# Performance work log

Measured on AMD Instinct MI355X. Metric: run time of the kernel, lower is better.

Reference implementation:

```python
import jax, jax.numpy as jnp
import numpy as np

B, S, DIM, NH = 2, 2048, 1536, 12
HD = DIM // NH            # 128
C = HD // 2               # 64 rotary pairs
CF = C - 2 * (C // 3)     # 22 (frame axis)
CH = C // 3               # 21 (height axis)
CW = C // 3               # 21 (width axis)
GF, GH, GW = 8, 16, 16    # grid sizes, GF*GH*GW == S
EPS = 1e-6


def _freq_table(n_pos, dim):
    inv = 1.0 / (10000.0 ** (np.arange(dim, dtype=np.float64) / dim))
    ang = np.outer(np.arange(n_pos, dtype=np.float64), inv)
    return (np.cos(ang).astype(np.float32), np.sin(ang).astype(np.float32))


def setup_inputs() -> dict:
    key = jax.random.key(0)
    ks = jax.random.split(key, 8)
    scale = 0.02
    cos_f, sin_f = _freq_table(GF, CF)
    cos_h, sin_h = _freq_table(GH, CH)
    cos_w, sin_w = _freq_table(GW, CW)
    return {
        'x': jax.random.normal(ks[0], (B, S, DIM), dtype=jnp.float32),
        'seq_lens': jnp.array([2048, 1600], dtype=jnp.int32),
        'f': GF, 'h': GH, 'w': GW,
        'wq': scale * jax.random.normal(ks[1], (DIM, DIM), dtype=jnp.float32),
        'bq': jnp.zeros((DIM,), jnp.float32),
        'wk': scale * jax.random.normal(ks[2], (DIM, DIM), dtype=jnp.float32),
        'bk': jnp.zeros((DIM,), jnp.float32),
        'wv': scale * jax.random.normal(ks[3], (DIM, DIM), dtype=jnp.float32),
        'bv': jnp.zeros((DIM,), jnp.float32),
        'wo': scale * jax.random.normal(ks[4], (DIM, DIM), dtype=jnp.float32),
        'bo': jnp.zeros((DIM,), jnp.float32),
        'nq_w': jnp.ones((DIM,), jnp.float32),
        'nk_w': jnp.ones((DIM,), jnp.float32),
        'cos_f': jnp.asarray(cos_f), 'sin_f': jnp.asarray(sin_f),
        'cos_h': jnp.asarray(cos_h), 'sin_h': jnp.asarray(sin_h),
        'cos_w': jnp.asarray(cos_w), 'sin_w': jnp.asarray(sin_w),
    }


def _rmsnorm(t, wt):
    return t * jax.lax.rsqrt(jnp.mean(t * t, axis=-1, keepdims=True) + EPS) * wt


def _grid_rope(t, cos, sin, b, s):
    # t: [b, s, NH, HD] ; cos/sin: [s, 1, C] (per-position assembled freqs)
    tp = t.reshape(b, s, NH, C, 2)
    xr, xi = tp[..., 0], tp[..., 1]
    rr = xr * cos - xi * sin          # complex multiply by e^{i*theta}
    ri = xr * sin + xi * cos
    return jnp.stack([rr, ri], axis=-1).reshape(b, s, NH, HD)


def reference(x, seq_lens, f, h, w, wq, bq, wk, bk, wv, bv, wo, bo,
              nq_w, nk_w, cos_f, sin_f, cos_h, sin_h, cos_w, sin_w):
    b, s, _ = x.shape
    # QKV projections with RMSNorm on q/k over full dim (as in the module)
    q = _rmsnorm(x @ wq.T + bq, nq_w).reshape(b, s, NH, HD)
    k = _rmsnorm(x @ wk.T + bk, nk_w).reshape(b, s, NH, HD)
    v = (x @ wv.T + bv).reshape(b, s, NH, HD)
    # grid-indexed RoPE: zero offsets / target==grid => arange sampling per axis
    idx = jnp.arange(s)
    fi = idx // (h * w)
    hi = (idx // w) % h
    wi = idx % w
    cos = jnp.concatenate([cos_f[fi], cos_h[hi], cos_w[wi]], axis=-1)[:, None, :]
    sin = jnp.concatenate([sin_f[fi], sin_h[hi], sin_w[wi]], axis=-1)[:, None, :]
    qr = _grid_rope(q, cos, sin, b, s)
    kr = _grid_rope(k, cos, sin, b, s)
    # attention with ragged key-length masking (flash_attention k_lens)
    scale = 1.0 / jnp.sqrt(jnp.float32(HD))
    scores = jnp.einsum('bqnd,bknd->bnqk', qr, kr) * scale
    kmask = idx[None, :] < seq_lens[:, None]            # [b, s]
    scores = jnp.where(kmask[:, None, None, :], scores, jnp.float32(-1e30))
    attn = jax.nn.softmax(scores, axis=-1)
    out = jnp.einsum('bnqk,bknd->bqnd', attn, v).reshape(b, s, DIM)
    return out @ wo.T + bo
```

## Files before the change

### kernel.cpp

```cpp
#include <hip/hip_runtime.h>
#include <hip/hip_bf16.h>
#include <math.h>

#define DIM_  1536
#define NH_   12
#define HD_   128
#define S_    2048
#define B_    2
#define M_    (B_*S_)
#define WEL_  (DIM_*DIM_)

typedef __attribute__((ext_vector_type(8))) _Float16 f16x8;
typedef __attribute__((ext_vector_type(4))) short short4v;
typedef __attribute__((ext_vector_type(8))) short short8v;
typedef __attribute__((ext_vector_type(4))) float f32x4;

#define SSCALE_LOG2E (0.08838834764831845f * 1.4426950408889634f)

static __device__ __forceinline__ short f2h(float f) {
  union { _Float16 h; short s; } u;
  u.h = (_Float16)f;
  return u.s;
}

static __device__ __forceinline__ unsigned pk2h(float a, float b) {
  typedef __attribute__((ext_vector_type(2))) __fp16 fp16x2;
  union { fp16x2 v; unsigned u; } u2;
  u2.v = __builtin_amdgcn_cvt_pkrtz(a, b);
  return u2.u;
}

__global__ __launch_bounds__(256) void f2h_k(
    const float* __restrict__ in, short* __restrict__ out, int n8)
{
  int i = blockIdx.x * 256 + threadIdx.x;
  if (i >= n8) return;
  const float4* p = (const float4*)in + (size_t)i * 2;
  float4 a = p[0], b = p[1];
  short8v o;
  o[0] = f2h(a.x); o[1] = f2h(a.y); o[2] = f2h(a.z); o[3] = f2h(a.w);
  o[4] = f2h(b.x); o[5] = f2h(b.y); o[6] = f2h(b.z); o[7] = f2h(b.w);
  *((short8v*)out + i) = o;
}

__global__ __launch_bounds__(256) void f2h4_k(
    const float* __restrict__ x, const float* __restrict__ wq,
    const float* __restrict__ wk, const float* __restrict__ wv,
    short* __restrict__ x16, short* __restrict__ w16)
{
  int i = blockIdx.x * 256 + threadIdx.x;
  const float* src; short* dst; int j;
  if (i < 786432)       { src = x;  dst = x16;            j = i; }
  else if (i < 1081344) { src = wq; dst = w16;            j = i - 786432; }
  else if (i < 1376256) { src = wk; dst = w16 + WEL_;     j = i - 1081344; }
  else                  { src = wv; dst = w16 + 2 * WEL_; j = i - 1376256; }
  const float4* p = (const float4*)src + (size_t)j * 2;
  float4 a = p[0], b = p[1];
  short8v o;
  o[0] = f2h(a.x); o[1] = f2h(a.y); o[2] = f2h(a.z); o[3] = f2h(a.w);
  o[4] = f2h(b.x); o[5] = f2h(b.y); o[6] = f2h(b.z); o[7] = f2h(b.w);
  *((short8v*)dst + j) = o;
}

template<int MODE>
static __device__ __forceinline__ void gemm16_core(
    const short* __restrict__ A16, const short* __restrict__ W16,
    const float* __restrict__ bias, short* __restrict__ Outp,
    int m0, int n0)
{
  __shared__ __align__(16) char Atile[8192];
  __shared__ __align__(16) char Btile[8192];
  const int tid = threadIdx.x;
  const int l  = tid & 63, w = tid >> 6;
  const int wr = w >> 1, wc = w & 1;
  const int lc = l & 15, lg = l >> 4;

  f32x4 acc[4][4] = {};

  const int rs  = w * 16 + (l >> 2);
  const int gsl = ((l & 3) ^ ((rs >> 1) & 3)) * 8;
  const short* gA0 = A16 + (size_t)(m0 + rs) * DIM_ + gsl;
  const short* gA1 = A16 + (size_t)(m0 + 64 + rs) * DIM_ + gsl;
  const short* gB0 = W16 + (size_t)(n0 + rs) * DIM_ + gsl;
  const short* gB1 = W16 + (size_t)(n0 + 64 + rs) * DIM_ + gsl;

  for (int k0 = 0; k0 < DIM_; k0 += 32) {
    __builtin_amdgcn_global_load_lds(
        (const __attribute__((address_space(1))) unsigned*)(gA0 + k0),
        (__attribute__((address_space(3))) unsigned*)(Atile + w * 1024), 16, 0, 0);
    __builtin_amdgcn_global_load_lds(
        (const __attribute__((address_space(1))) unsigned*)(gA1 + k0),
        (__attribute__((address_space(3))) unsigned*)(Atile + 4096 + w * 1024), 16, 0, 0);
    __builtin_amdgcn_global_load_lds(
        (const __attribute__((address_space(1))) unsigned*)(gB0 + k0),
        (__attribute__((address_space(3))) unsigned*)(Btile + w * 1024), 16, 0, 0);
    __builtin_amdgcn_global_load_lds(
        (const __attribute__((address_space(1))) unsigned*)(gB1 + k0),
        (__attribute__((address_space(3))) unsigned*)(Btile + 4096 + w * 1024), 16, 0, 0);
    __syncthreads();

    f16x8 af[4], bf[4];
#pragma unroll
    for (int mt = 0; mt < 4; ++mt) {
      int ar = wr * 64 + mt * 16 + lc;
      af[mt] = *(const f16x8*)(Atile + ar * 64 + ((lg ^ ((ar >> 1) & 3)) << 4));
    }
#pragma unroll
    for (int nt = 0; nt < 4; ++nt) {
      int br = wc * 64 + nt * 16 + lc;
      bf[nt] = *(const f16x8*)(Btile + br * 64 + ((lg ^ ((br >> 1) & 3)) << 4));
    }
#pragma unroll
    for (int mt = 0; mt < 4; ++mt)
#pragma unroll
      for (int nt = 0; nt < 4; ++nt)
        acc[mt][nt] = __builtin_amdgcn_mfma_f32_16x16x32_f16(af[mt], bf[nt], acc[mt][nt], 0, 0, 0);
    __syncthreads();
  }

  if (MODE == 0) {
#pragma unroll
    for (int nt = 0; nt < 4; ++nt) {
      int col = n0 + wc * 64 + nt * 16 + lc;
      float bb = bias[col];
#pragma unroll
      for (int mt = 0; mt < 4; ++mt) {
#pragma unroll
        for (int r = 0; r < 4; ++r) {
          int rowm = m0 + wr * 64 + mt * 16 + lg * 4 + r;
          Outp[(size_t)rowm * DIM_ + col] = f2h(acc[mt][nt][r] + bb);
        }
      }
    }
  } else {
#pragma unroll
    for (int nt = 0; nt < 4; ++nt) {
      int colg = n0 + wc * 64 + nt * 16 + lc;
      int h = colg >> 7, d = colg & 127;
      float bb = bias[colg];
#pragma unroll
      for (int mt = 0; mt < 4; ++mt) {
        int rowg = m0 + wr * 64 + mt * 16 + lg * 4;
        int b = rowg >> 11, s = rowg & (S_ - 1);
        short4v o4;
#pragma unroll
        for (int r = 0; r < 4; ++r) o4[r] = f2h(acc[mt][nt][r] + bb);
        *(short4v*)(Outp + ((size_t)((b * NH_ + h) * HD_ + d)) * S_ + s) = o4;
      }
    }
  }
}

__global__ __launch_bounds__(256) void gemm_qkv16_k(
    const short* __restrict__ x16, const short* __restrict__ w16,
    const float* __restrict__ bq, const float* __restrict__ bk,
    const float* __restrict__ bv,
    short* __restrict__ q16, short* __restrict__ k16, short* __restrict__ vt)
{
  const int z = blockIdx.z;
  if (z == 2)
    gemm16_core<2>(x16, w16 + 2 * (size_t)WEL_, bv, vt,
                   blockIdx.y * 128, blockIdx.x * 128);
  else
    gemm16_core<0>(x16, w16 + (size_t)z * WEL_, z ? bk : bq, z ? k16 : q16,
                   blockIdx.y * 128, blockIdx.x * 128);
}

__global__ __launch_bounds__(256) void gemm_out64_k(
    const short* __restrict__ att16, const short* __restrict__ wo16,
    const float* __restrict__ bo, float* __restrict__ out)
{
  __shared__ __align__(16) char Atile[8192];
  __shared__ __align__(16) char Btile[4096];
  const int m0 = blockIdx.y * 128, n0 = blockIdx.x * 64;
  const int tid = threadIdx.x;
  const int l  = tid & 63, w = tid >> 6;
  const int lc = l & 15, lg = l >> 4;

  f32x4 acc[2][4] = {};

  const int rsA = w * 32 + (l >> 2);
  const int rsB = w * 16 + (l >> 2);
  const int gslA = ((l & 3) ^ ((rsA >> 1) & 3)) * 8;
  const int gslB = ((l & 3) ^ ((rsB >> 1) & 3)) * 8;
  const short* gA0 = att16 + (size_t)(m0 + rsA) * DIM_ + gslA;
  const short* gA1 = att16 + (size_t)(m0 + 16 + rsA) * DIM_ + gslA;
  const short* gB0 = wo16 + (size_t)(n0 + rsB) * DIM_ + gslB;

  for (int k0 = 0; k0 < DIM_; k0 += 32) {
    __builtin_amdgcn_global_load_lds(
        (const __attribute__((address_space(1))) unsigned*)(gA0 + k0),
        (__attribute__((address_space(3))) unsigned*)(Atile + w * 2048), 16, 0, 0);
    __builtin_amdgcn_global_load_lds(
        (const __attribute__((address_space(1))) unsigned*)(gA1 + k0),
        (__attribute__((address_space(3))) unsigned*)(Atile + w * 2048 + 1024), 16, 0, 0);
    __builtin_amdgcn_global_load_lds(
        (const __attribute__((address_space(1))) unsigned*)(gB0 + k0),
        (__attribute__((address_space(3))) unsigned*)(Btile + w * 1024), 16, 0, 0);
    __syncthreads();

    f16x8 af[2], bf[4];
#pragma unroll
    for (int mt = 0; mt < 2; ++mt) {
      int ar = w * 32 + mt * 16 + lc;
      af[mt] = *(const f16x8*)(Atile + ar * 64 + ((lg ^ ((ar >> 1) & 3)) << 4));
    }
#pragma unroll
    for (int nt = 0; nt < 4; ++nt) {
      int br = nt * 16 + lc;
      bf[nt] = *(const f16x8*)(Btile + br * 64 + ((lg ^ ((br >> 1) & 3)) << 4));
    }
#pragma unroll
    for (int mt = 0; mt < 2; ++mt)
#pragma unroll
      for (int nt = 0; nt < 4; ++nt)
        acc[mt][nt] = __builtin_amdgcn_mfma_f32_16x16x32_f16(af[mt], bf[nt], acc[mt][nt], 0, 0, 0);
    __syncthreads();
  }

#pragma unroll
  for (int nt = 0; nt < 4; ++nt) {
    int col = n0 + nt * 16 + lc;
    float bb = bo[col];
#pragma unroll
    for (int mt = 0; mt < 2; ++mt) {
#pragma unroll
      for (int r = 0; r < 4; ++r) {
        int rowm = m0 + w * 32 + mt * 16 + lg * 4 + r;
        out[(size_t)rowm * DIM_ + col] = acc[mt][nt][r] + bb;
      }
    }
  }
}

__global__ __launch_bounds__(256) void rms_rope_pack16_k(
    const short* __restrict__ t, const float* __restrict__ w,
    const float* __restrict__ cf, const float* __restrict__ sf,
    const float* __restrict__ ch, const float* __restrict__ sh,
    const float* __restrict__ cw, const float* __restrict__ sw,
    short* __restrict__ outb, float qsc)
{
  const int row = blockIdx.x;
  const int b   = row >> 11;
  const int s   = row & (S_ - 1);
  const _Float16* rp = (const _Float16*)(t + (size_t)row * DIM_);

  float ss = 0.f;
  for (int i = threadIdx.x; i < DIM_; i += 256) {
    float v2 = (float)rp[i]; ss += v2 * v2;
  }
#pragma unroll
  for (int off = 32; off > 0; off >>= 1) ss += __shfl_down(ss, off);
  __shared__ float red[4];
  if ((threadIdx.x & 63) == 0) red[threadIdx.x >> 6] = ss;
  __syncthreads();
  float scale = rsqrtf((red[0] + red[1] + red[2] + red[3]) * (1.f / DIM_) + 1e-6f) * qsc;

  const int fi = s >> 8;
  const int hi = (s >> 4) & 15;
  const int wi = s & 15;

  for (int p = threadIdx.x; p < NH_ * 64; p += 256) {
    int n = p >> 6, c = p & 63;
    float co, si;
    if (c < 22)      { co = cf[fi * 22 + c];        si = sf[fi * 22 + c]; }
    else if (c < 43) { co = ch[hi * 21 + (c - 22)]; si = sh[hi * 21 + (c - 22)]; }
    else             { co = cw[wi * 21 + (c - 43)]; si = sw[wi * 21 + (c - 43)]; }
    int d0 = n * HD_ + 2 * c;
    float xr = (float)rp[d0]     * scale * w[d0];
    float xi = (float)rp[d0 + 1] * scale * w[d0 + 1];
    float rr = xr * co - xi * si;
    float ri = xr * si + xi * co;
    *(unsigned int*)(outb + (((size_t)(b * NH_ + n) * S_ + s) * HD_ + 2 * c)) = pk2h(rr, ri);
  }
}

__global__ __launch_bounds__(256) void attn_mfma5_k(
    const short* __restrict__ qb, const short* __restrict__ kb,
    const short* __restrict__ vtb, const int* __restrict__ seq_lens,
    short* __restrict__ o16)
{
  const int bh = blockIdx.y;
  const int b  = bh / NH_;
  const int h  = bh - b * NH_;
  const int q0 = blockIdx.x << 6;
  const int kvlen = seq_lens[b];
  const int tid  = threadIdx.x;
  const int wid  = tid >> 6;
  const int lane = tid & 63;
  const int lg   = lane >> 4;
  const int lc   = lane & 15;
  const int xo   = (lc & 7) << 4;

  __shared__ __align__(16) char Kt[16384];
  __shared__ __align__(16) char Vt[16384];
  __shared__ __align__(16) char Pt[4][2048];

  f16x8 bq[4];
  {
    const size_t base = ((size_t)bh * S_ + q0 + wid * 16 + lc) * HD_;
#pragma unroll
    for (int dc = 0; dc < 4; ++dc)
      bq[dc] = *(const f16x8*)(qb + base + dc * 32 + lg * 8);
  }

  const short* kgA = kb + ((size_t)bh * S_ + wid * 16 + lg) * HD_
                        + ((lc * 8) ^ (lg << 3));
  const short* kgB = kb + ((size_t)bh * S_ + wid * 16 + 4 + lg) * HD_
                        + ((lc * 8) ^ ((lg ^ 4) << 3));
  const short* vg  = vtb + ((size_t)bh * HD_ + wid * 32 + (lane >> 3)) * S_
                         + (((lane & 7) * 8) ^ ((lane >> 3) << 3));

#define STAGE_K()                                                              \
  {                                                                            \
    _Pragma("unroll")                                                          \
    for (int j = 0; j < 4; ++j) {                                              \
      const short* g = (j & 1) ? (kgB + ((j - 1) >> 1) * (8 * HD_))            \
                               : (kgA + (j >> 1) * (8 * HD_));                 \
      __builtin_amdgcn_global_load_lds(                                        \
          (const __attribute__((address_space(1))) unsigned*)g,                \
          (__attribute__((address_space(3))) unsigned*)(Kt + (wid * 16 + j * 4) * 256), \
          16, 0, 0);                                                           \
    }                                                                          \
  }
#define STAGE_V()                                                              \
  {                                                                            \
    _Pragma("unroll")                                                          \
    for (int j = 0; j < 4; ++j) {                                              \
      __builtin_amdgcn_global_load_lds(                                        \
          (const __attribute__((address_space(1))) unsigned*)(vg + j * 8 * S_),\
          (__attribute__((address_space(3))) unsigned*)(Vt + (wid * 32 + j * 8) * 128), \
          16, 0, 0);                                                           \
    }                                                                          \
  }

  f32x4 oacc[8] = {};
  float m = -3.0e38f, l = 0.f;

  const int nt = kvlen >> 6;

  STAGE_K();
  kgA += 64 * HD_; kgB += 64 * HD_;
  __syncthreads();

  for (int ti = 0; ti < nt; ++ti) {
    STAGE_V();
    vg += 64;

    f32x4 s[4];
    __builtin_amdgcn_s_setprio(1);
#pragma unroll
    for (int kt = 0; kt < 4; ++kt) {
      f32x4 a = {0.f, 0.f, 0.f, 0.f};
      const char* kr = Kt + (kt * 16 + lc) * 256;
#pragma unroll
      for (int dc = 0; dc < 4; ++dc) {
        f16x8 kf = *(const f16x8*)(kr + ((dc * 64 + lg * 16) ^ xo));
        a = __builtin_amdgcn_mfma_f32_16x16x32_f16(kf, bq[dc], a, 0, 0, 0);
      }
      s[kt] = a;
    }
    __builtin_amdgcn_s_setprio(0);

    float t0 = -3.0e38f;
#pragma unroll
    for (int kt = 0; kt < 4; ++kt)
#pragma unroll
      for (int r = 0; r < 4; ++r) t0 = fmaxf(t0, s[kt][r]);
    t0 = fmaxf(t0, __shfl_xor(t0, 16));
    t0 = fmaxf(t0, __shfl_xor(t0, 32));

    if (__any(t0 > m + 8.f)) {
      float mn = fmaxf(m, t0);
      float a  = exp2f(m - mn);
      m = mn; l *= a;
#pragma unroll
      for (int r = 0; r < 4; ++r) {
        float ar = __shfl(a, 4 * lg + r);
#pragma unroll
        for (int n = 0; n < 8; ++n) oacc[n][r] *= ar;
      }
    }
    float ls = 0.f;
#pragma unroll
    for (int kt = 0; kt < 4; ++kt)
#pragma unroll
      for (int r = 0; r < 4; ++r) {
        float p = exp2f(s[kt][r] - m); s[kt][r] = p; ls += p;
      }
    ls += __shfl_xor(ls, 16);
    ls += __shfl_xor(ls, 32);
    l += ls;

    {
      char* pr = Pt[wid] + lc * 128;
#pragma unroll
      for (int kt = 0; kt < 4; ++kt) {
#pragma unroll
        for (int rr = 0; rr < 2; ++rr) {
          unsigned u = pk2h(s[kt][2 * rr], s[kt][2 * rr + 1]);
          int off = (kt * 32 + lg * 8 + rr * 4) ^ xo;
          *(unsigned*)(pr + off) = u;
        }
      }
    }

    __syncthreads();

    if (ti + 1 < nt) {
      STAGE_K();
      kgA += 64 * HD_; kgB += 64 * HD_;
    }

    __builtin_amdgcn_s_setprio(1);
#pragma unroll
    for (int kc = 0; kc < 2; ++kc) {
      f16x8 pa = *(const f16x8*)(Pt[wid] + lc * 128 + ((kc * 64 + lg * 16) ^ xo));
#pragma unroll
      for (int n = 0; n < 8; ++n) {
        f16x8 vf = *(const f16x8*)(Vt + (n * 16 + lc) * 128 + ((kc * 64 + lg * 16) ^ xo));
        oacc[n] = __builtin_amdgcn_mfma_f32_16x16x32_f16(pa, vf, oacc[n], 0, 0, 0);
      }
    }
    __builtin_amdgcn_s_setprio(0);

    __syncthreads();
  }

#pragma unroll
  for (int r = 0; r < 4; ++r) {
    float li = 1.f / __shfl(l, 4 * lg + r);
    int qrow = q0 + wid * 16 + 4 * lg + r;
#pragma unroll
    for (int n = 0; n < 8; ++n)
      o16[((size_t)(b * S_ + qrow) * NH_ + h) * HD_ + n * 16 + lc] = f2h(oacc[n][r] * li);
  }
#undef STAGE_K
#undef STAGE_V
}

extern "C" void kernel_launch(void* const* d_in, const int* in_sizes, int n_in,
                              void* d_out, int out_size, void* d_ws, size_t ws_size,
                              hipStream_t stream) {
  const float* x        = (const float*)d_in[0];
  const int*   seq_lens = (const int*)d_in[1];
  const float* wq = (const float*)d_in[5];
  const float* bq = (const float*)d_in[6];
  const float* wk = (const float*)d_in[7];
  const float* bk = (const float*)d_in[8];
  const float* wv = (const float*)d_in[9];
  const float* bv = (const float*)d_in[10];
  const float* wo = (const float*)d_in[11];
  const float* bo = (const float*)d_in[12];
  const float* nq = (const float*)d_in[13];
  const float* nk = (const float*)d_in[14];
  const float* cf = (const float*)d_in[15];
  const float* sf = (const float*)d_in[16];
  const float* ch = (const float*)d_in[17];
  const float* sh = (const float*)d_in[18];
  const float* cw = (const float*)d_in[19];
  const float* sw = (const float*)d_in[20];

  const size_t rowelems = (size_t)M_ * DIM_;
  short* x16 = (short*)d_ws;
  short* w16 = x16 + rowelems;
  short* q16 = w16 + 3 * (size_t)WEL_;
  short* k16 = q16 + rowelems;
  short* vt  = k16 + rowelems;
  short* qh  = vt + rowelems;
  short* kh  = qh + rowelems;
  short* att16 = q16;
  short* wo16  = k16;
  float* out = (float*)d_out;

  f2h4_k<<<6528, 256, 0, stream>>>(x, wq, wk, wv, x16, w16);

  gemm_qkv16_k<<<dim3(DIM_ / 128, M_ / 128, 3), 256, 0, stream>>>(
      x16, w16, bq, bk, bv, q16, k16, vt);

  rms_rope_pack16_k<<<M_, 256, 0, stream>>>(q16, nq, cf, sf, ch, sh, cw, sw, qh,
                                            SSCALE_LOG2E);
  rms_rope_pack16_k<<<M_, 256, 0, stream>>>(k16, nk, cf, sf, ch, sh, cw, sw, kh, 1.0f);

  f2h_k<<<1152, 256, 0, stream>>>(wo, wo16, WEL_ / 8);

  attn_mfma5_k<<<dim3(S_ / 64, B_ * NH_), 256, 0, stream>>>(qh, kh, vt, seq_lens, att16);

  gemm_out64_k<<<dim3(DIM_ / 64, M_ / 128), 256, 0, stream>>>(att16, wo16, bo, out);
}
```

Baseline: 257.0 us.

## Double-buffer LDS tiles in GEMM kernels and fold wo conversion into one launch

Both the QKV and output-projection GEMMs now keep two LDS buffers and prefetch the next K-slice while MFMAs run on the current one. The MFMA block is wrapped in s_setprio to favour math issue. The separate wo fp16 conversion kernel is merged into the combined conversion launch, and wo16 gets its own workspace slot instead of reusing k16. This hides global-load latency and removes one launch, at the cost of doubled LDS per block, which may lower occupancy, and a larger workspace.

```diff
diff --git a/kernel.cpp b/kernel.cpp
--- a/kernel.cpp
+++ b/kernel.cpp
@@ -30,30 +30,19 @@
   return u2.u;
 }
 
-__global__ __launch_bounds__(256) void f2h_k(
-    const float* __restrict__ in, short* __restrict__ out, int n8)
-{
-  int i = blockIdx.x * 256 + threadIdx.x;
-  if (i >= n8) return;
-  const float4* p = (const float4*)in + (size_t)i * 2;
-  float4 a = p[0], b = p[1];
-  short8v o;
-  o[0] = f2h(a.x); o[1] = f2h(a.y); o[2] = f2h(a.z); o[3] = f2h(a.w);
-  o[4] = f2h(b.x); o[5] = f2h(b.y); o[6] = f2h(b.z); o[7] = f2h(b.w);
-  *((short8v*)out + i) = o;
-}
-
-__global__ __launch_bounds__(256) void f2h4_k(
+__global__ __launch_bounds__(256) void f2h5_k(
     const float* __restrict__ x, const float* __restrict__ wq,
     const float* __restrict__ wk, const float* __restrict__ wv,
-    short* __restrict__ x16, short* __restrict__ w16)
+    const float* __restrict__ wo,
+    short* __restrict__ x16, short* __restrict__ w16, short* __restrict__ wo16)
 {
   int i = blockIdx.x * 256 + threadIdx.x;
   const float* src; short* dst; int j;
   if (i < 786432)       { src = x;  dst = x16;            j = i; }
   else if (i < 1081344) { src = wq; dst = w16;            j = i - 786432; }
   else if (i < 1376256) { src = wk; dst = w16 + WEL_;     j = i - 1081344; }
-  else                  { src = wv; dst = w16 + 2 * WEL_; j = i - 1376256; }
+  else if (i < 1671168) { src = wv; dst = w16 + 2 * WEL_; j = i - 1376256; }
+  else                  { src = wo; dst = wo16;           j = i - 1671168; }
   const float4* p = (const float4*)src + (size_t)j * 2;
   float4 a = p[0], b = p[1];
   short8v o;
@@ -66,10 +55,8 @@
 static __device__ __forceinline__ void gemm16_core(
     const short* __restrict__ A16, const short* __restrict__ W16,
     const float* __restrict__ bias, short* __restrict__ Outp,
-    int m0, int n0)
+    int m0, int n0, char* __restrict__ Ab, char* __restrict__ Bb)
 {
-  __shared__ __align__(16) char Atile[8192];
-  __shared__ __align__(16) char Btile[8192];
   const int tid = threadIdx.x;
   const int l  = tid & 63, w = tid >> 6;
   const int wr = w >> 1, wc = w & 1;
@@ -84,39 +71,51 @@
   const short* gB0 = W16 + (size_t)(n0 + rs) * DIM_ + gsl;
   const short* gB1 = W16 + (size_t)(n0 + 64 + rs) * DIM_ + gsl;
 
+#define GSTAGE(buf, k0)                                                        \
+  {                                                                            \
+    __builtin_amdgcn_global_load_lds(                                          \
+        (const __attribute__((address_space(1))) unsigned*)(gA0 + (k0)),       \
+        (__attribute__((address_space(3))) unsigned*)(Ab + (buf) * 8192 + w * 1024), 16, 0, 0); \
+    __builtin_amdgcn_global_load_lds(                                          \
+        (const __attribute__((address_space(1))) unsigned*)(gA1 + (k0)),       \
+        (__attribute__((address_space(3))) unsigned*)(Ab + (buf) * 8192 + 4096 + w * 1024), 16, 0, 0); \
+    __builtin_amdgcn_global_load_lds(                                          \
+        (const __attribute__((address_space(1))) unsigned*)(gB0 + (k0)),       \
+        (__attribute__((address_space(3))) unsigned*)(Bb + (buf) * 8192 + w * 1024), 16, 0, 0); \
+    __builtin_amdgcn_global_load_lds(                                          \
+        (const __attribute__((address_space(1))) unsigned*)(gB1 + (k0)),       \
+        (__attribute__((address_space(3))) unsigned*)(Bb + (buf) * 8192 + 4096 + w * 1024), 16, 0, 0); \
+  }
+
+  GSTAGE(0, 0);
+  __syncthreads();
+  int cur = 0;
   for (int k0 = 0; k0 < DIM_; k0 += 32) {
-    __builtin_amdgcn_global_load_lds(
-        (const __attribute__((address_space(1))) unsigned*)(gA0 + k0),
-        (__attribute__((address_space(3))) unsigned*)(Atile + w * 1024), 16, 0, 0);
-    __builtin_amdgcn_global_load_lds(
-        (const __attribute__((address_space(1))) unsigned*)(gA1 + k0),
-        (__attribute__((address_space(3))) unsigned*)(Atile + 4096 + w * 1024), 16, 0, 0);
-    __builtin_amdgcn_global_load_lds(
-        (const __attribute__((address_space(1))) unsigned*)(gB0 + k0),
-        (__attribute__((address_space(3))) unsigned*)(Btile + w * 1024), 16, 0, 0);
-    __builtin_amdgcn_global_load_lds(
-        (const __attribute__((address_space(1))) unsigned*)(gB1 + k0),
-        (__attribute__((address_space(3))) unsigned*)(Btile + 4096 + w * 1024), 16, 0, 0);
-    __syncthreads();
-
+    const char* Ac = Ab + cur * 8192;
+    const char* Bc = Bb + cur * 8192;
     f16x8 af[4], bf[4];
 #pragma unroll
     for (int mt = 0; mt < 4; ++mt) {
       int ar = wr * 64 + mt * 16 + lc;
-      af[mt] = *(const f16x8*)(Atile + ar * 64 + ((lg ^ ((ar >> 1) & 3)) << 4));
+      af[mt] = *(const f16x8*)(Ac + ar * 64 + ((lg ^ ((ar >> 1) & 3)) << 4));
     }
 #pragma unroll
     for (int nt = 0; nt < 4; ++nt) {
       int br = wc * 64 + nt * 16 + lc;
-      bf[nt] = *(const f16x8*)(Btile + br * 64 + ((lg ^ ((br >> 1) & 3)) << 4));
-    }
+      bf[nt] = *(const f16x8*)(Bc + br * 64 + ((lg ^ ((br >> 1) & 3)) << 4));
+    }
+    if (k0 + 32 < DIM_) GSTAGE(cur ^ 1, k0 + 32);
+    __builtin_amdgcn_s_setprio(1);
 #pragma unroll
     for (int mt = 0; mt < 4; ++mt)
 #pragma unroll
       for (int nt = 0; nt < 4; ++nt)
         acc[mt][nt] = __builtin_amdgcn_mfma_f32_16x16x32_f16(af[mt], bf[nt], acc[mt][nt], 0, 0, 0);
+    __builtin_amdgcn_s_setprio(0);
     __syncthreads();
-  }
+    cur ^= 1;
+  }
+#undef GSTAGE
 
   if (MODE == 0) {
 #pragma unroll
@@ -157,21 +156,23 @@
     const float* __restrict__ bv,
     short* __restrict__ q16, short* __restrict__ k16, short* __restrict__ vt)
 {
+  __shared__ __align__(16) char Ab[2][8192];
+  __shared__ __align__(16) char Bb[2][8192];
   const int z = blockIdx.z;
   if (z == 2)
     gemm16_core<2>(x16, w16 + 2 * (size_t)WEL_, bv, vt,
-                   blockIdx.y * 128, blockIdx.x * 128);
+                   blockIdx.y * 128, blockIdx.x * 128, &Ab[0][0], &Bb[0][0]);
   else
     gemm16_core<0>(x16, w16 + (size_t)z * WEL_, z ? bk : bq, z ? k16 : q16,
-                   blockIdx.y * 128, blockIdx.x * 128);
+                   blockIdx.y * 128, blockIdx.x * 128, &Ab[0][0], &Bb[0][0]);
 }
 
 __global__ __launch_bounds__(256) void gemm_out64_k(
     const short* __restrict__ att16, const short* __restrict__ wo16,
     const float* __restrict__ bo, float* __restrict__ out)
 {
-  __shared__ __align__(16) char Atile[8192];
-  __shared__ __align__(16) char Btile[4096];
+  __shared__ __align__(16) char Ab[2][8192];
+  __shared__ __align__(16) char Bb[2][4096];
   const int m0 = blockIdx.y * 128, n0 = blockIdx.x * 64;
   const int tid = threadIdx.x;
   const int l  = tid & 63, w = tid >> 6;
@@ -187,36 +188,48 @@
   const short* gA1 = att16 + (size_t)(m0 + 16 + rsA) * DIM_ + gslA;
   const short* gB0 = wo16 + (size_t)(n0 + rsB) * DIM_ + gslB;
 
+#define GSTAGE(buf, k0)                                                        \
+  {                                                                            \
+    __builtin_amdgcn_global_load_lds(                                          \
+        (const __attribute__((address_space(1))) unsigned*)(gA0 + (k0)),       \
+        (__attribute__((address_space(3))) unsigned*)(&Ab[buf][0] + w * 2048), 16, 0, 0); \
+    __builtin_amdgcn_global_load_lds(                                          \
+        (const __attribute__((address_space(1))) unsigned*)(gA1 + (k0)),       \
+        (__attribute__((address_space(3))) unsigned*)(&Ab[buf][0] + w * 2048 + 1024), 16, 0, 0); \
+    __builtin_amdgcn_global_load_lds(                                          \
+        (const __attribute__((address_space(1))) unsigned*)(gB0 + (k0)),       \
+        (__attribute__((address_space(3))) unsigned*)(&Bb[buf][0] + w * 1024), 16, 0, 0); \
+  }
+
+  GSTAGE(0, 0);
+  __syncthreads();
+  int cur = 0;
   for (int k0 = 0; k0 < DIM_; k0 += 32) {
-    __builtin_amdgcn_global_load_lds(
-        (const __attribute__((address_space(1))) unsigned*)(gA0 + k0),
-        (__attribute__((address_space(3))) unsigned*)(Atile + w * 2048), 16, 0, 0);
-    __builtin_amdgcn_global_load_lds(
-        (const __attribute__((address_space(1))) unsigned*)(gA1 + k0),
-        (__attribute__((address_space(3))) unsigned*)(Atile + w * 2048 + 1024), 16, 0, 0);
-    __builtin_amdgcn_global_load_lds(
-        (const __attribute__((address_space(1))) unsigned*)(gB0 + k0),
-        (__attribute__((address_space(3))) unsigned*)(Btile + w * 1024), 16, 0, 0);
-    __syncthreads();
-
+    const char* Ac = &Ab[cur][0];
+    const char* Bc = &Bb[cur][0];
     f16x8 af[2], bf[4];
 #pragma unroll
     for (int mt = 0; mt < 2; ++mt) {
       int ar = w * 32 + mt * 16 + lc;
-      af[mt] = *(const f16x8*)(Atile + ar * 64 + ((lg ^ ((ar >> 1) & 3)) << 4));
+      af[mt] = *(const f16x8*)(Ac + ar * 64 + ((lg ^ ((ar >> 1) & 3)) << 4));
     }
 #pragma unroll
     for (int nt = 0; nt < 4; ++nt) {
       int br = nt * 16 + lc;
-      bf[nt] = *(const f16x8*)(Btile + br * 64 + ((lg ^ ((br >> 1) & 3)) << 4));
-    }
+      bf[nt] = *(const f16x8*)(Bc + br * 64 + ((lg ^ ((br >> 1) & 3)) << 4));
+    }
+    if (k0 + 32 < DIM_) GSTAGE(cur ^ 1, k0 + 32);
+    __builtin_amdgcn_s_setprio(1);
 #pragma unroll
     for (int mt = 0; mt < 2; ++mt)
 #pragma unroll
       for (int nt = 0; nt < 4; ++nt)
         acc[mt][nt] = __builtin_amdgcn_mfma_f32_16x16x32_f16(af[mt], bf[nt], acc[mt][nt], 0, 0, 0);
+    __builtin_amdgcn_s_setprio(0);
     __syncthreads();
-  }
+    cur ^= 1;
+  }
+#undef GSTAGE
 
 #pragma unroll
   for (int nt = 0; nt < 4; ++nt) {
@@ -462,18 +475,18 @@
   const float* sw = (const float*)d_in[20];
 
   const size_t rowelems = (size_t)M_ * DIM_;
-  short* x16 = (short*)d_ws;
-  short* w16 = x16 + rowelems;
-  short* q16 = w16 + 3 * (size_t)WEL_;
-  short* k16 = q16 + rowelems;
-  short* vt  = k16 + rowelems;
-  short* qh  = vt + rowelems;
-  short* kh  = qh + rowelems;
+  short* x16  = (short*)d_ws;
+  short* w16  = x16 + rowelems;
+  short* wo16 = w16 + 3 * (size_t)WEL_;
+  short* q16  = wo16 + WEL_;
+  short* k16  = q16 + rowelems;
+  short* vt   = k16 + rowelems;
+  short* qh   = vt + rowelems;
+  short* kh   = qh + rowelems;
   short* att16 = q16;
-  short* wo16  = k16;
   float* out = (float*)d_out;
 
-  f2h4_k<<<6528, 256, 0, stream>>>(x, wq, wk, wv, x16, w16);
+  f2h5_k<<<7680, 256, 0, stream>>>(x, wq, wk, wv, wo, x16, w16, wo16);
 
   gemm_qkv16_k<<<dim3(DIM_ / 128, M_ / 128, 3), 256, 0, stream>>>(
       x16, w16, bq, bk, bv, q16, k16, vt);
@@ -482,8 +495,6 @@
                                             SSCALE_LOG2E);
   rms_rope_pack16_k<<<M_, 256, 0, stream>>>(k16, nk, cf, sf, ch, sh, cw, sw, kh, 1.0f);
 
-  f2h_k<<<1152, 256, 0, stream>>>(wo, wo16, WEL_ / 8);
-
   attn_mfma5_k<<<dim3(S_ / 64, B_ * NH_), 256, 0, stream>>>(qh, kh, vt, seq_lens, att16);
 
   gemm_out64_k<<<dim3(DIM_ / 64, M_ / 128), 256, 0, stream>>>(att16, wo16, bo, out);
```

Result: faster. 248.8 us (-3.2%).
